# Performance work log

Measured on AMD Instinct MI355X. Metric: run time of the kernel, lower is better.

The kernel has to match this reference:

```python
import jax, jax.numpy as jnp
import numpy as np

NUM_HEADS = 16
ROPE_BASE = 10000.0
MAX_POS = 4096


def _rope_tables(head_dim):
    inv_freq = 1.0 / (ROPE_BASE ** (np.arange(0, head_dim, 2, dtype=np.float32) / head_dim))
    freqs = np.arange(MAX_POS, dtype=np.float32)[:, None] * inv_freq[None, :]
    emb = np.concatenate([freqs, freqs], axis=-1)  # [MAX_POS, head_dim]
    return jnp.asarray(np.cos(emb)), jnp.asarray(np.sin(emb))


def _rotate_half(x):
    d = x.shape[-1] // 2
    return jnp.concatenate([-x[..., d:], x[..., :d]], axis=-1)


def _apply_rope(x, pos, cos_t, sin_t):
    # x: [B,H,S,D], pos: [B,S]
    cos = cos_t[pos][:, None]  # [B,1,S,D]
    sin = sin_t[pos][:, None]
    return x * cos + _rotate_half(x) * sin


def setup_inputs() -> dict:
    key = jax.random.key(0)
    ks = jax.random.split(key, 8)
    B, N, M, C = 2, 2048, 2048, 1024
    s = 1.0 / np.sqrt(C)
    return {
        "query": jax.random.normal(ks[0], (B, N, C), jnp.float32),
        "key": jax.random.normal(ks[1], (B, M, C), jnp.float32),
        "query_pos": jnp.broadcast_to(jnp.arange(N, dtype=jnp.int32), (B, N)),
        "key_pos": jnp.broadcast_to(jnp.arange(M, dtype=jnp.int32), (B, M)),
        "Wq": jax.random.normal(ks[2], (C, C), jnp.float32) * s,
        "bq": jnp.zeros((C,), jnp.float32),
        "Wk": jax.random.normal(ks[3], (C, C), jnp.float32) * s,
        "Wv": jax.random.normal(ks[4], (C, C), jnp.float32) * s,
        "bv": jnp.zeros((C,), jnp.float32),
        "Wo": jax.random.normal(ks[5], (C, C), jnp.float32) * s,
        "bo": jnp.zeros((C,), jnp.float32),
    }


def reference(query, key, query_pos, key_pos, Wq, bq, Wk, Wv, bv, Wo, bo):
    B, N, C = query.shape
    M = key.shape[1]
    H = NUM_HEADS
    D = C // H
    scale = D ** -0.5
    cos_t, sin_t = _rope_tables(D)

    value = key  # value defaults to key
    identity = query

    q = (query @ Wq.T + bq).reshape(B, N, H, D).transpose(0, 2, 1, 3)
    k = (key @ Wk.T).reshape(B, M, H, D).transpose(0, 2, 1, 3)
    v = (value @ Wv.T + bv).reshape(B, M, H, D).transpose(0, 2, 1, 3)

    q = _apply_rope(q, query_pos, cos_t, sin_t)
    k = _apply_rope(k, key_pos, cos_t, sin_t)

    attn = jnp.einsum('bhnd,bhmd->bhnm', q, k) * scale
    attn = jax.nn.softmax(attn, axis=-1)
    x = jnp.einsum('bhnm,bhmd->bhnd', attn, v)  # [B,H,N,D]
    x = x.transpose(0, 2, 1, 3).reshape(B, N, C)
    x = x @ Wo.T + bo
    return x + identity
```

## Files before the change

### kernel.cpp

```cpp
#include <hip/hip_runtime.h>
#include <hip/hip_bf16.h>
#include <stdint.h>

#define B_ 2
#define N_ 2048
#define M_ 2048
#define C_ 1024
#define H_ 16
#define D_ 64

typedef __attribute__((ext_vector_type(8))) short s16x8;
typedef __attribute__((ext_vector_type(4))) short s16x4;
typedef __attribute__((ext_vector_type(4))) float f32x4;
typedef __attribute__((ext_vector_type(16))) float f32x16;

__device__ __attribute__((always_inline)) inline short f2b(float f){
    __hip_bfloat16 h = __float2bfloat16(f); short s; __builtin_memcpy(&s, &h, 2); return s;
}
__device__ __attribute__((always_inline)) inline float b2f(short s){
    __hip_bfloat16 h; __builtin_memcpy(&h, &s, 2); return __bfloat162float(h);
}

#define MFMA16(a,b,c) __builtin_amdgcn_mfma_f32_16x16x32_bf16(a,b,c,0,0,0)
#define MFMA32(a,b,c) __builtin_amdgcn_mfma_f32_32x32x16_bf16(a,b,c,0,0,0)

__device__ __attribute__((always_inline)) inline void gl_lds16(const void* g, void* l){
    __builtin_amdgcn_global_load_lds((__attribute__((address_space(1))) void*)g,
                                     (__attribute__((address_space(3))) void*)l, 16, 0, 0);
}
__device__ __attribute__((always_inline)) inline unsigned fbits(float f){
    unsigned u; __builtin_memcpy(&u, &f, 4); return u;
}
__device__ __attribute__((always_inline)) inline unsigned cvtpk(float lo, float hi){
    unsigned r;
    asm("v_cvt_pk_bf16_f32 %0, %1, %2" : "=v"(r) : "v"(lo), "v"(hi));
    return r;
}
__device__ __attribute__((always_inline)) inline void lane32swap(unsigned &a, unsigned &b){
    asm("v_permlane32_swap_b32 %0, %1" : "+v"(a), "+v"(b));
}

__global__ void cvt_all(const float* __restrict__ q, const float* __restrict__ k,
                        const float* __restrict__ wq, const float* __restrict__ wk,
                        const float* __restrict__ wv, const float* __restrict__ wo,
                        short* __restrict__ dst){
    long i = ((long)blockIdx.x * 256 + threadIdx.x) * 8;
    const float* src; long off;
    if      (i <  4194304L){ src = q;  off = i; }
    else if (i <  8388608L){ src = k;  off = i - 4194304L; }
    else if (i <  9437184L){ src = wq; off = i - 8388608L; }
    else if (i < 10485760L){ src = wk; off = i - 9437184L; }
    else if (i < 11534336L){ src = wv; off = i - 10485760L; }
    else                   { src = wo; off = i - 11534336L; }
    float4 a = *(const float4*)(src + off);
    float4 b = *(const float4*)(src + off + 4);
    s16x8 o;
    o[0]=f2b(a.x); o[1]=f2b(a.y); o[2]=f2b(a.z); o[3]=f2b(a.w);
    o[4]=f2b(b.x); o[5]=f2b(b.y); o[6]=f2b(b.z); o[7]=f2b(b.w);
    *(s16x8*)(dst + i) = o;
}

__global__ __launch_bounds__(256, 3) void gemm_qkv(
    const short* __restrict__ qbf, const short* __restrict__ kbf,
    const short* __restrict__ W,
    const float* __restrict__ bq, const float* __restrict__ bv,
    const int* __restrict__ kpos,
    short* __restrict__ qproj, short* __restrict__ kproj, short* __restrict__ vT)
{
    __shared__ short As[128 * 32];
    __shared__ short Bs[128 * 32];
    const int n0 = blockIdx.x * 128, m0 = blockIdx.y * 128;
    const int sel = n0 >> 10;
    const short* A = (sel == 0) ? qbf : kbf;
    const int tid = threadIdx.x, lane = tid & 63, wave = tid >> 6;
    const int quad = lane >> 4, l16 = lane & 15;
    const int wr = (wave >> 1) * 64, wc = (wave & 1) * 64;
    const int srow = lane >> 2, scol = (lane & 3) * 8;

    f32x4 acc[4][4] = {};

    const short* Ag = A + (size_t)(m0 + wave * 32 + srow) * C_ + scol;
    const short* Bg = W + (size_t)(n0 + wave * 32 + srow) * C_ + scol;
    short* lA0 = As + (wave * 32) * 32;
    short* lA1 = As + (wave * 32 + 16) * 32;
    short* lB0 = Bs + (wave * 32) * 32;
    short* lB1 = Bs + (wave * 32 + 16) * 32;

    for (int k0 = 0; k0 < C_; k0 += 32){
        __syncthreads();
        gl_lds16(Ag + k0, lA0);
        gl_lds16(Ag + k0 + 16 * (size_t)C_, lA1);
        gl_lds16(Bg + k0, lB0);
        gl_lds16(Bg + k0 + 16 * (size_t)C_, lB1);
        __syncthreads();
        s16x8 af[4], bfr[4];
        #pragma unroll
        for (int t = 0; t < 4; t++) af[t]  = *(const s16x8*)&As[(wr + t*16 + l16) * 32 + quad * 8];
        #pragma unroll
        for (int t = 0; t < 4; t++) bfr[t] = *(const s16x8*)&Bs[(wc + t*16 + l16) * 32 + quad * 8];
        #pragma unroll
        for (int i = 0; i < 4; i++)
            #pragma unroll
            for (int j = 0; j < 4; j++)
                acc[i][j] = MFMA16(af[i], bfr[j], acc[i][j]);
    }

    if (sel == 0){
        #pragma unroll
        for (int j = 0; j < 4; j++){
            int c = n0 + wc + j * 16 + l16;
            float bb = bq[c];
            #pragma unroll
            for (int i = 0; i < 4; i++){
                int row = m0 + wr + i * 16 + quad * 4;
                #pragma unroll
                for (int r = 0; r < 4; r++)
                    qproj[(size_t)(row + r) * C_ + c] = f2b(acc[i][j][r] + bb);
            }
        }
    } else if (sel == 1){
        #pragma unroll
        for (int j2 = 0; j2 < 2; j2++){
            int c1 = n0 - 1024 + wc + j2 * 16 + l16;
            int irot = c1 & 63;
            float invf = exp2f((float)irot * (-13.287712379549449f / 32.0f));
            #pragma unroll
            for (int i = 0; i < 4; i++){
                int row = m0 + wr + i * 16 + quad * 4;
                #pragma unroll
                for (int r = 0; r < 4; r++){
                    float pos = (float)kpos[row + r];
                    float ang = pos * invf;
                    float cs = __cosf(ang), sn = __sinf(ang);
                    float x1 = acc[i][j2][r], x2 = acc[i][j2 + 2][r];
                    kproj[(size_t)(row + r) * C_ + c1]      = f2b(x1 * cs - x2 * sn);
                    kproj[(size_t)(row + r) * C_ + c1 + 32] = f2b(x2 * cs + x1 * sn);
                }
            }
        }
    } else {
        #pragma unroll
        for (int j = 0; j < 4; j++){
            int col = n0 - 2048 + wc + j * 16 + l16;
            int h = col >> 6, d = col & 63;
            float bb = bv[col];
            #pragma unroll
            for (int i = 0; i < 4; i++){
                int row = m0 + wr + i * 16 + quad * 4;
                int b = row >> 11, m = row & 2047;
                unsigned u0 = (unsigned)(unsigned short)f2b(acc[i][j][0] + bb) |
                              ((unsigned)(unsigned short)f2b(acc[i][j][1] + bb) << 16);
                unsigned u1 = (unsigned)(unsigned short)f2b(acc[i][j][2] + bb) |
                              ((unsigned)(unsigned short)f2b(acc[i][j][3] + bb) << 16);
                uint2 u; u.x = u0; u.y = u1;
                *(uint2*)&vT[(((size_t)(b * H_ + h)) * D_ + d) * M_ + m] = u;
            }
        }
    }
}

__global__ __launch_bounds__(256, 4) void gemm_out(
    const short* __restrict__ A, const short* __restrict__ W,
    const float* __restrict__ bias, const float* __restrict__ resid,
    float* __restrict__ outf)
{
    __shared__ short As[128 * 32];
    __shared__ short Bs[64 * 32];
    const int n0 = blockIdx.x * 64, m0 = blockIdx.y * 128;
    const int tid = threadIdx.x, lane = tid & 63, wave = tid >> 6;
    const int quad = lane >> 4, l16 = lane & 15;
    const int srow = lane >> 2, scol = (lane & 3) * 8;

    f32x4 acc[2][4] = {};
    const short* Ag = A + (size_t)(m0 + wave * 32 + srow) * C_ + scol;
    const short* Bg = W + (size_t)(n0 + wave * 16 + srow) * C_ + scol;
    short* lA0 = As + (wave * 32) * 32;
    short* lA1 = As + (wave * 32 + 16) * 32;
    short* lB  = Bs + (wave * 16) * 32;

    for (int k0 = 0; k0 < C_; k0 += 32){
        __syncthreads();
        gl_lds16(Ag + k0, lA0);
        gl_lds16(Ag + k0 + 16 * (size_t)C_, lA1);
        gl_lds16(Bg + k0, lB);
        __syncthreads();
        s16x8 af[2], bfr[4];
        #pragma unroll
        for (int t = 0; t < 2; t++) af[t]  = *(const s16x8*)&As[(wave*32 + t*16 + l16) * 32 + quad * 8];
        #pragma unroll
        for (int t = 0; t < 4; t++) bfr[t] = *(const s16x8*)&Bs[(t*16 + l16) * 32 + quad * 8];
        #pragma unroll
        for (int i = 0; i < 2; i++)
            #pragma unroll
            for (int j = 0; j < 4; j++)
                acc[i][j] = MFMA16(af[i], bfr[j], acc[i][j]);
    }

    #pragma unroll
    for (int j = 0; j < 4; j++){
        int c = n0 + j * 16 + l16;
        float bb = bias[c];
        #pragma unroll
        for (int i = 0; i < 2; i++){
            int row = m0 + wave * 32 + i * 16 + quad * 4;
            #pragma unroll
            for (int r = 0; r < 4; r++){
                size_t idx = (size_t)(row + r) * C_ + c;
                outf[idx] = acc[i][j][r] + bb + resid[idx];
            }
        }
    }
}

__global__ __launch_bounds__(512, 4) void flash_attn(
    const short* __restrict__ q, const short* __restrict__ k,
    const short* __restrict__ vt, short* __restrict__ o,
    const int* __restrict__ qpos)
{
    __shared__ short smem[17920];
    const int b = blockIdx.y >> 4, h = blockIdx.y & 15;
    const int n0 = blockIdx.x * 128;
    const int tid = threadIdx.x, lane = tid & 63, wave = tid >> 6;
    const int hi = lane >> 5, l32 = lane & 31;
    const int wq = wave & 3, kq = wave >> 2;

    s16x8 qf[4];
    const float fac = 0.18033688011112042f;
    {
        int qrow = n0 + wq * 32 + l32;
        const short* qg = &q[((size_t)(b * N_ + qrow)) * C_ + h * D_];
        float pos = (float)qpos[b * N_ + qrow];
        s16x8 raw[4];
        #pragma unroll
        for (int c = 0; c < 4; c++) raw[c] = *(const s16x8*)&qg[c * 16 + hi * 8];
        #pragma unroll
        for (int c = 0; c < 2; c++){
            s16x8 olo, ohi8;
            #pragma unroll
            for (int j = 0; j < 8; j++){
                int irot = c * 16 + hi * 8 + j;
                float invf = exp2f((float)irot * (-13.287712379549449f / 32.0f));
                float ang = pos * invf;
                float cs = __cosf(ang), sn = __sinf(ang);
                float x1 = b2f(raw[c][j]), x2 = b2f(raw[c + 2][j]);
                olo[j]  = f2b((x1 * cs - x2 * sn) * fac);
                ohi8[j] = f2b((x2 * cs + x1 * sn) * fac);
            }
            qf[c] = olo; qf[c + 2] = ohi8;
        }
    }

    const short* kg = k  + (size_t)(b * M_) * C_ + h * D_;
    const short* vg = vt + ((size_t)(b * H_ + h)) * D_ * M_;
    const int srow0 = tid >> 3, sseg = (tid & 7) * 8;

    union V8 { s16x8 v; uint2 u[2]; };
    V8 kreg, vreg;

    kreg.v = *(const s16x8*)&kg[(size_t)srow0 * C_ + sseg];
    vreg.v = *(const s16x8*)&vg[(size_t)srow0 * M_ + sseg];
    {
        short* kd = &smem[srow0 * 68 + sseg];
        *(uint2*)kd = kreg.u[0]; *(uint2*)(kd + 4) = kreg.u[1];
        short* vd = &smem[8704 + srow0 * 68 + sseg];
        *(uint2*)vd = vreg.u[0]; *(uint2*)(vd + 4) = vreg.u[1];
    }

    f32x16 zero16 = {};
    f32x16 oacc[2] = {zero16, zero16};
    float lacc = 0.f;

    for (int st = 0; st < 32; st++){
        const int p = st & 1;
        __syncthreads();
        if (st < 31){
            kreg.v = *(const s16x8*)&kg[((size_t)((st + 1) * 64 + srow0)) * C_ + sseg];
            vreg.v = *(const s16x8*)&vg[(size_t)srow0 * M_ + (st + 1) * 64 + sseg];
        }
        const short* Kp = &smem[p * 4352];
        const short* Vp = &smem[8704 + p * 4352];

        s16x4 kf[4][2];
        #pragma unroll
        for (int c = 0; c < 4; c++){
            const short* a = &Kp[(kq * 32 + l32) * 68 + c * 16 + hi * 8];
            kf[c][0] = *(const s16x4*)a; kf[c][1] = *(const s16x4*)(a + 4);
        }
        s16x8 vf[2][2];
        #pragma unroll
        for (int dt = 0; dt < 2; dt++)
            #pragma unroll
            for (int c = 0; c < 2; c++){
                const short* a = &Vp[(dt * 32 + l32) * 68 + kq * 32 + c * 16 + hi * 8];
                vf[dt][c] = __builtin_shufflevector(*(const s16x4*)a, *(const s16x4*)(a + 4),
                                                    0,1,2,3,4,5,6,7);
            }

        f32x16 sv = {};
        #pragma unroll
        for (int c = 0; c < 4; c++){
            s16x8 ka = __builtin_shufflevector(kf[c][0], kf[c][1], 0,1,2,3,4,5,6,7);
            sv = MFMA32(ka, qf[c], sv);
        }
        float pe[16];
        #pragma unroll
        for (int e = 0; e < 16; e++) pe[e] = __builtin_amdgcn_exp2f(sv[e]);
        float ls = 0.f;
        #pragma unroll
        for (int e = 0; e < 16; e += 4) ls += (pe[e] + pe[e+1]) + (pe[e+2] + pe[e+3]);
        lacc += ls;
        s16x8 pf[2];
        #pragma unroll
        for (int c = 0; c < 2; c++){
            unsigned a1 = cvtpk(pe[8*c + 0], pe[8*c + 1]);
            unsigned a2 = cvtpk(pe[8*c + 2], pe[8*c + 3]);
            unsigned b1 = cvtpk(pe[8*c + 4], pe[8*c + 5]);
            unsigned b2 = cvtpk(pe[8*c + 6], pe[8*c + 7]);
            lane32swap(a1, b1);
            lane32swap(a2, b2);
            union { unsigned u[4]; s16x8 v; } pk;
            pk.u[0] = a1; pk.u[1] = a2; pk.u[2] = b1; pk.u[3] = b2;
            pf[c] = pk.v;
        }

        #pragma unroll
        for (int dt = 0; dt < 2; dt++)
            #pragma unroll
            for (int c = 0; c < 2; c++)
                oacc[dt] = MFMA32(pf[c], vf[dt][c], oacc[dt]);

        if (st < 31){
            int pn = p ^ 1;
            short* kd = &smem[pn * 4352 + srow0 * 68 + sseg];
            *(uint2*)kd = kreg.u[0]; *(uint2*)(kd + 4) = kreg.u[1];
            short* vd = &smem[8704 + pn * 4352 + srow0 * 68 + sseg];
            *(uint2*)vd = vreg.u[0]; *(uint2*)(vd + 4) = vreg.u[1];
        }
    }

    __syncthreads();

    float* LO   = (float*)smem;
    float* Lsum = (float*)&smem[17408];
    float* Linv = Lsum + 128;

    float l0 = lacc + __shfl_xor(lacc, 32);

    if (kq == 1){
        Lsum[wq * 32 + l32] = l0;
        #pragma unroll
        for (int dt = 0; dt < 2; dt++)
            #pragma unroll
            for (int e = 0; e < 16; e++){
                int qrow = wq * 32 + (e & 3) + 8 * (e >> 2) + 4 * hi;
                LO[qrow * 65 + dt * 32 + l32] = oacc[dt][e];
            }
    }
    __syncthreads();
    if (kq == 0){
        float lt = l0 + Lsum[wq * 32 + l32];
        Linv[wq * 32 + l32] = 1.0f / lt;
        asm volatile("s_waitcnt lgkmcnt(0)" ::: "memory");
        #pragma unroll
        for (int dt = 0; dt < 2; dt++)
            #pragma unroll
            for (int e = 0; e < 16; e++){
                int qrow = wq * 32 + (e & 3) + 8 * (e >> 2) + 4 * hi;
                float val = (oacc[dt][e] + LO[qrow * 65 + dt * 32 + l32]) * Linv[qrow];
                o[((size_t)(b * N_ + n0 + qrow)) * C_ + h * D_ + dt * 32 + l32] = f2b(val);
            }
    }
}

extern "C" void kernel_launch(void* const* d_in, const int* in_sizes, int n_in,
                              void* d_out, int out_size, void* d_ws, size_t ws_size,
                              hipStream_t stream) {
    const float* query = (const float*)d_in[0];
    const float* key   = (const float*)d_in[1];
    const int*   qpos  = (const int*)d_in[2];
    const int*   kpos  = (const int*)d_in[3];
    const float* Wq    = (const float*)d_in[4];
    const float* bq    = (const float*)d_in[5];
    const float* Wk    = (const float*)d_in[6];
    const float* Wv    = (const float*)d_in[7];
    const float* bv    = (const float*)d_in[8];
    const float* Wo    = (const float*)d_in[9];
    const float* bo    = (const float*)d_in[10];
    float* out = (float*)d_out;

    const size_t E4M = (size_t)4 * 1024 * 1024;
    const size_t E1M = (size_t)1024 * 1024;
    short* ws    = (short*)d_ws;
    short* qbf   = ws;
    short* kbf   = qbf   + E4M;
    short* wqkvb = kbf   + E4M;
    short* wob   = wqkvb + 3 * E1M;
    short* qproj = wob   + E1M;
    short* kproj = qproj + E4M;
    short* vT    = kproj + E4M;
    short* attn  = qbf;

    cvt_all<<<6144, 256, 0, stream>>>(query, key, Wq, Wk, Wv, Wo, ws);

    gemm_qkv<<<dim3(24, 32), 256, 0, stream>>>(qbf, kbf, wqkvb, bq, bv, kpos,
                                               qproj, kproj, vT);

    flash_attn<<<dim3(16, 32), 512, 0, stream>>>(qproj, kproj, vT, attn, qpos);

    gemm_out<<<dim3(16, 32), 256, 0, stream>>>(attn, wob, bo, query, out);
}
```

Measured before the change: 206.9 us.

## Load K/V fragments directly from global into registers and remap blocks for XCD locality

The flash attention kernel stops staging K and V tiles through double-buffered shared memory. Each wave now loads its MFMA fragments straight from global memory into registers and prefetches the next tile between the two matmul phases, which removes the per-iteration barrier and the LDS traffic. The launch also becomes a 1D grid with a remapped block id, so blocks for the same batch/head are likely to sit on the same XCD and share L2. The cost is that every wave issues its own uncoalesced global loads and duplicates K/V reads across the four query waves, relying on the cache to absorb them.

```diff
diff --git a/kernel.cpp b/kernel.cpp
--- a/kernel.cpp
+++ b/kernel.cpp
@@ -27,9 +27,6 @@
 __device__ __attribute__((always_inline)) inline void gl_lds16(const void* g, void* l){
     __builtin_amdgcn_global_load_lds((__attribute__((address_space(1))) void*)g,
                                      (__attribute__((address_space(3))) void*)l, 16, 0, 0);
-}
-__device__ __attribute__((always_inline)) inline unsigned fbits(float f){
-    unsigned u; __builtin_memcpy(&u, &f, 4); return u;
 }
 __device__ __attribute__((always_inline)) inline unsigned cvtpk(float lo, float hi){
     unsigned r;
@@ -217,9 +214,15 @@
     const short* __restrict__ vt, short* __restrict__ o,
     const int* __restrict__ qpos)
 {
-    __shared__ short smem[17920];
-    const int b = blockIdx.y >> 4, h = blockIdx.y & 15;
-    const int n0 = blockIdx.x * 128;
+    __shared__ float sLO[128 * 65];
+    __shared__ float sL[256];
+
+    const int bid = blockIdx.x;
+    const int wgid = (bid & 7) * 64 + (bid >> 3);
+    const int y = wgid >> 4, x = wgid & 15;
+    const int b = y >> 4, h = y & 15;
+    const int n0 = x * 128;
+
     const int tid = threadIdx.x, lane = tid & 63, wave = tid >> 6;
     const int hi = lane >> 5, l32 = lane & 31;
     const int wq = wave & 3, kq = wave >> 2;
@@ -252,70 +255,49 @@
 
     const short* kg = k  + (size_t)(b * M_) * C_ + h * D_;
     const short* vg = vt + ((size_t)(b * H_ + h)) * D_ * M_;
-    const int srow0 = tid >> 3, sseg = (tid & 7) * 8;
-
-    union V8 { s16x8 v; uint2 u[2]; };
-    V8 kreg, vreg;
-
-    kreg.v = *(const s16x8*)&kg[(size_t)srow0 * C_ + sseg];
-    vreg.v = *(const s16x8*)&vg[(size_t)srow0 * M_ + sseg];
-    {
-        short* kd = &smem[srow0 * 68 + sseg];
-        *(uint2*)kd = kreg.u[0]; *(uint2*)(kd + 4) = kreg.u[1];
-        short* vd = &smem[8704 + srow0 * 68 + sseg];
-        *(uint2*)vd = vreg.u[0]; *(uint2*)(vd + 4) = vreg.u[1];
-    }
+    const int krow = kq * 32 + l32;
+    const int col8 = hi * 8;
+
+    s16x8 kf[4], vf[2][2];
+    #pragma unroll
+    for (int c = 0; c < 4; c++)
+        kf[c] = *(const s16x8*)&kg[(size_t)krow * C_ + c * 16 + col8];
+    #pragma unroll
+    for (int dt = 0; dt < 2; dt++)
+        #pragma unroll
+        for (int c = 0; c < 2; c++)
+            vf[dt][c] = *(const s16x8*)&vg[(size_t)(dt * 32 + l32) * M_ + kq * 32 + c * 16 + col8];
 
     f32x16 zero16 = {};
     f32x16 oacc[2] = {zero16, zero16};
     float lacc = 0.f;
 
     for (int st = 0; st < 32; st++){
-        const int p = st & 1;
-        __syncthreads();
+        f32x16 sv = {};
+        #pragma unroll
+        for (int c = 0; c < 4; c++)
+            sv = MFMA32(kf[c], qf[c], sv);
+
         if (st < 31){
-            kreg.v = *(const s16x8*)&kg[((size_t)((st + 1) * 64 + srow0)) * C_ + sseg];
-            vreg.v = *(const s16x8*)&vg[(size_t)srow0 * M_ + (st + 1) * 64 + sseg];
-        }
-        const short* Kp = &smem[p * 4352];
-        const short* Vp = &smem[8704 + p * 4352];
-
-        s16x4 kf[4][2];
-        #pragma unroll
-        for (int c = 0; c < 4; c++){
-            const short* a = &Kp[(kq * 32 + l32) * 68 + c * 16 + hi * 8];
-            kf[c][0] = *(const s16x4*)a; kf[c][1] = *(const s16x4*)(a + 4);
-        }
-        s16x8 vf[2][2];
-        #pragma unroll
-        for (int dt = 0; dt < 2; dt++)
-            #pragma unroll
-            for (int c = 0; c < 2; c++){
-                const short* a = &Vp[(dt * 32 + l32) * 68 + kq * 32 + c * 16 + hi * 8];
-                vf[dt][c] = __builtin_shufflevector(*(const s16x4*)a, *(const s16x4*)(a + 4),
-                                                    0,1,2,3,4,5,6,7);
-            }
-
-        f32x16 sv = {};
-        #pragma unroll
-        for (int c = 0; c < 4; c++){
-            s16x8 ka = __builtin_shufflevector(kf[c][0], kf[c][1], 0,1,2,3,4,5,6,7);
-            sv = MFMA32(ka, qf[c], sv);
-        }
-        float pe[16];
-        #pragma unroll
-        for (int e = 0; e < 16; e++) pe[e] = __builtin_amdgcn_exp2f(sv[e]);
+            #pragma unroll
+            for (int c = 0; c < 4; c++)
+                kf[c] = *(const s16x8*)&kg[(size_t)((st + 1) * 64 + krow) * C_ + c * 16 + col8];
+        }
+
+        #pragma unroll
+        for (int e = 0; e < 16; e++) sv[e] = __builtin_amdgcn_exp2f(sv[e]);
         float ls = 0.f;
         #pragma unroll
-        for (int e = 0; e < 16; e += 4) ls += (pe[e] + pe[e+1]) + (pe[e+2] + pe[e+3]);
+        for (int e = 0; e < 16; e += 4) ls += (sv[e] + sv[e+1]) + (sv[e+2] + sv[e+3]);
         lacc += ls;
+
         s16x8 pf[2];
         #pragma unroll
         for (int c = 0; c < 2; c++){
-            unsigned a1 = cvtpk(pe[8*c + 0], pe[8*c + 1]);
-            unsigned a2 = cvtpk(pe[8*c + 2], pe[8*c + 3]);
-            unsigned b1 = cvtpk(pe[8*c + 4], pe[8*c + 5]);
-            unsigned b2 = cvtpk(pe[8*c + 6], pe[8*c + 7]);
+            unsigned a1 = cvtpk(sv[8*c + 0], sv[8*c + 1]);
+            unsigned a2 = cvtpk(sv[8*c + 2], sv[8*c + 3]);
+            unsigned b1 = cvtpk(sv[8*c + 4], sv[8*c + 5]);
+            unsigned b2 = cvtpk(sv[8*c + 6], sv[8*c + 7]);
             lane32swap(a1, b1);
             lane32swap(a2, b2);
             union { unsigned u[4]; s16x8 v; } pk;
@@ -330,43 +312,38 @@
                 oacc[dt] = MFMA32(pf[c], vf[dt][c], oacc[dt]);
 
         if (st < 31){
-            int pn = p ^ 1;
-            short* kd = &smem[pn * 4352 + srow0 * 68 + sseg];
-            *(uint2*)kd = kreg.u[0]; *(uint2*)(kd + 4) = kreg.u[1];
-            short* vd = &smem[8704 + pn * 4352 + srow0 * 68 + sseg];
-            *(uint2*)vd = vreg.u[0]; *(uint2*)(vd + 4) = vreg.u[1];
-        }
-    }
-
-    __syncthreads();
-
-    float* LO   = (float*)smem;
-    float* Lsum = (float*)&smem[17408];
-    float* Linv = Lsum + 128;
+            #pragma unroll
+            for (int dt = 0; dt < 2; dt++)
+                #pragma unroll
+                for (int c = 0; c < 2; c++)
+                    vf[dt][c] = *(const s16x8*)&vg[(size_t)(dt * 32 + l32) * M_ +
+                                                   (st + 1) * 64 + kq * 32 + c * 16 + col8];
+        }
+    }
 
     float l0 = lacc + __shfl_xor(lacc, 32);
 
     if (kq == 1){
-        Lsum[wq * 32 + l32] = l0;
+        sL[wq * 32 + l32] = l0;
         #pragma unroll
         for (int dt = 0; dt < 2; dt++)
             #pragma unroll
             for (int e = 0; e < 16; e++){
                 int qrow = wq * 32 + (e & 3) + 8 * (e >> 2) + 4 * hi;
-                LO[qrow * 65 + dt * 32 + l32] = oacc[dt][e];
+                sLO[qrow * 65 + dt * 32 + l32] = oacc[dt][e];
             }
     }
     __syncthreads();
     if (kq == 0){
-        float lt = l0 + Lsum[wq * 32 + l32];
-        Linv[wq * 32 + l32] = 1.0f / lt;
+        float lt = l0 + sL[wq * 32 + l32];
+        sL[128 + wq * 32 + l32] = 1.0f / lt;
         asm volatile("s_waitcnt lgkmcnt(0)" ::: "memory");
         #pragma unroll
         for (int dt = 0; dt < 2; dt++)
             #pragma unroll
             for (int e = 0; e < 16; e++){
                 int qrow = wq * 32 + (e & 3) + 8 * (e >> 2) + 4 * hi;
-                float val = (oacc[dt][e] + LO[qrow * 65 + dt * 32 + l32]) * Linv[qrow];
+                float val = (oacc[dt][e] + sLO[qrow * 65 + dt * 32 + l32]) * sL[128 + qrow];
                 o[((size_t)(b * N_ + n0 + qrow)) * C_ + h * D_ + dt * 32 + l32] = f2b(val);
             }
     }
@@ -405,7 +382,7 @@
     gemm_qkv<<<dim3(24, 32), 256, 0, stream>>>(qbf, kbf, wqkvb, bq, bv, kpos,
                                                qproj, kproj, vT);
 
-    flash_attn<<<dim3(16, 32), 512, 0, stream>>>(qproj, kproj, vT, attn, qpos);
+    flash_attn<<<512, 512, 0, stream>>>(qproj, kproj, vT, attn, qpos);
 
     gemm_out<<<dim3(16, 32), 256, 0, stream>>>(attn, wob, bo, query, out);
 }
```

After: 278.4 us. +34.6%, slower.
